# Kernel optimization log

Hardware: AMD Instinct MI355X
Metric: run time of the kernel (lower is better)

Reference implementation:

```python
import jax, jax.numpy as jnp
import numpy as np
import math

N = 20000          # nodes (residues)
E = 640000         # edges
CS = 384           # c_s
CZ = 128           # c_z
CH = 16            # c_hidden
H = 8              # no_heads
PQK = 8            # no_qk_points == no_v_points (forced equal, see notes)
FS = 128           # scalar channels in feat_irreps
PIN = 16           # vector channels in feat_irreps
HC = H * CH        # 128
HPQ = H * PQK * 3  # 192
CZ4 = CZ // 4      # 32
OUT_IN = HC + 3 * H + H + H * CZ4  # 416 actual concat width
INF = 100000.0
EPS = 1e-8


def setup_inputs() -> dict:
    key = jax.random.key(0)
    ks = jax.random.split(key, 16)
    w = lambda k, i, o: (jax.random.normal(k, (i, o), jnp.float32) / np.float32(np.sqrt(i)))
    frame_s = jax.random.normal(ks[0], (N, CS), jnp.float32)
    tfn_t = jax.random.normal(ks[1], (N, FS + 3 * PIN), jnp.float32)
    z = jax.random.normal(ks[2], (E, CZ), jnp.float32)
    edge_index = jax.random.randint(ks[3], (2, E), 0, N)
    mask = jnp.ones((N,), jnp.float32)
    # Rigid transforms: proper-ish rotations via QR, translations
    rot, _ = jnp.linalg.qr(jax.random.normal(ks[4], (N, 3, 3), jnp.float32))
    trans = jax.random.normal(ks[5], (N, 3), jnp.float32)
    return {
        "frame_s": frame_s, "tfn_t": tfn_t, "z": z,
        "edge_index": edge_index, "mask": mask,
        "rot": rot, "trans": trans,
        "Wq": w(ks[6], CS, HC), "bq": jnp.zeros((HC,), jnp.float32),
        "Wk_s": w(ks[7], FS, HC), "Wk_v": w(ks[8], PIN, PQK),
        "Wqp": w(ks[9], CS, HPQ), "bqp": jnp.zeros((HPQ,), jnp.float32),
        "Wb": w(ks[10], CZ, H), "bb": jnp.zeros((H,), jnp.float32),
        "Wdz": w(ks[11], CZ, CZ4), "bdz": jnp.zeros((CZ4,), jnp.float32),
        # ipa_point_weights_init_: softplus(hw) == 1  =>  hw = log(e - 1)
        "head_weights": jnp.full((H,), np.float32(np.log(np.e - 1.0))),
        "Wout": w(ks[12], OUT_IN, CS), "bout": jnp.zeros((CS,), jnp.float32),
    }


def _segment_softmax(a, seg, n):
    # pyg-style numerically stable segment softmax over edges grouped by seg
    m = jax.ops.segment_max(a, seg, num_segments=n)
    m = jnp.where(jnp.isfinite(m), m, 0.0)
    e = jnp.exp(a - m[seg])
    s = jax.ops.segment_sum(e, seg, num_segments=n)
    return e / (s[seg] + 1e-16)


def _forward(frame_s, tfn_t, z, mask, rot, trans,
             Wq, bq, Wk_s, Wk_v, Wqp, bqp, Wb, bb, Wdz, bdz,
             head_weights, Wout, bout, edge_index):
    n = frame_s.shape[0]
    src = edge_index[1]
    dst = edge_index[0]

    # scalar queries: [N,H,C]
    q = (frame_s @ Wq + bq).reshape(n, H, CH)

    # o3.Linear (feat_irreps -> k_irreps): scalars mix scalars, vectors mix vectors.
    # NOTE: original code uses linear_k for BOTH k and v (faithful bug), so v==k.
    scal = tfn_t[:, :FS]
    vecs = tfn_t[:, FS:].reshape(n, PIN, 3)
    k_scal = scal @ Wk_s                                   # [N, HC]
    k_vec = jnp.einsum('npx,pq->nqx', vecs, Wk_v)          # [N, PQK, 3]
    k = k_scal.reshape(n, H, CH)
    v = k
    k_tail = k_vec.reshape(n, PQK * 3)                     # [N, 24]
    # torch: split([3]*PQK) then stack(dim=-1) -> [N,3,PQK], then view [N,H,-1,3]
    k_pts = jnp.stack(jnp.split(k_tail, PQK, axis=-1), axis=-1)  # [N,3,PQK]
    k_pts = k_pts.reshape(n, H, -1, 3)                     # [N,H,1,3]
    v_pts = k_pts

    # query points, rigid-transformed: [N,H,PQK,3]
    q_pts = frame_s @ Wqp + bqp                            # [N, 3*H*PQK]
    q_pts = jnp.stack(jnp.split(q_pts, 3, axis=-1), axis=-1)  # [N, H*PQK, 3]
    q_pts = jnp.einsum('nij,npj->npi', rot, q_pts) + trans[:, None, :]
    q_pts = q_pts.reshape(n, H, PQK, 3)

    # scalar attention logits [E,H]
    a = jnp.einsum('ehc,ehc->eh', q[src], k[dst])
    a = a * np.float32(math.sqrt(1.0 / (3 * CH)))
    b = z @ Wb + bb                                        # [E,H]
    a = a + np.float32(math.sqrt(1.0 / 3)) * b

    # point attention: disp [E,H,PQK,3] (k_pts broadcasts over points)
    disp = q_pts[src] - k_pts[dst]
    pt_att = jnp.sum(disp * disp, axis=-1)                 # [E,H,PQK]
    hw = jax.nn.softplus(head_weights) * np.float32(math.sqrt(1.0 / (3 * (PQK * 9.0 / 2))))
    pt_att = -0.5 * jnp.sum(pt_att * hw[None, :, None], axis=-1)  # [E,H]

    edge_mask = INF * (mask[dst] * mask[src] - 1.0)        # [E]
    a = a + pt_att + edge_mask[:, None]

    a = _segment_softmax(a, src, n)                        # [E,H]

    # scalar output
    o = jax.ops.segment_sum(a[..., None] * v[dst], src, num_segments=n)  # [N,H,C]
    o = o.reshape(n, HC)

    # point output
    o_pt = jax.ops.segment_sum(a[:, :, None, None] * v_pts[dst], src, num_segments=n)  # [N,H,1,3]
    o_pt = jnp.einsum('nji,nhpj->nhpi', rot, o_pt - trans[:, None, None, :])  # invert_apply
    o_pt_norm = jnp.sqrt(jnp.sum(o_pt * o_pt, axis=-1) + EPS).reshape(n, H)
    o_pt = o_pt.reshape(n, -1, 3)                          # [N,H,3]

    # pair output
    pair_z = z @ Wdz + bdz                                 # [E,CZ4]
    o_pair = jax.ops.segment_sum(a[..., None] * pair_z[:, None, :], src, num_segments=n)  # [N,H,CZ4]
    o_pair = o_pair.reshape(n, H * CZ4)

    feats = jnp.concatenate(
        [o, o_pt[..., 0], o_pt[..., 1], o_pt[..., 2], o_pt_norm, o_pair], axis=-1)  # [N,416]
    return feats @ Wout + bout                             # [N, CS]


def reference(frame_s, tfn_t, z, edge_index, mask, rot, trans,
              Wq, bq, Wk_s, Wk_v, Wqp, bqp, Wb, bb, Wdz, bdz,
              head_weights, Wout, bout):
    return _forward(frame_s, tfn_t, z, mask, rot, trans,
                    Wq, bq, Wk_s, Wk_v, Wqp, bqp, Wb, bb, Wdz, bdz,
                    head_weights, Wout, bout, edge_index)
```

## Files before the change

### kernel.cpp

```cpp
#include <hip/hip_runtime.h>
#include <math.h>

typedef __attribute__((ext_vector_type(8))) short short8;
typedef __attribute__((ext_vector_type(4))) float f32x4;

static __device__ inline unsigned short f2bf(float f) {
    union { float f; unsigned u; } v; v.f = f;
    unsigned r = v.u + 0x7FFF + ((v.u >> 16) & 1);
    return (unsigned short)(r >> 16);
}

template<int WJ, bool GATHER>
__global__ __launch_bounds__(256) void gemm_mfma(
    const float* __restrict__ A, int lda,
    const int* __restrict__ gidx,
    const float* __restrict__ BT, int ldb,
    const float* __restrict__ bias,
    float* __restrict__ C, int ldc,
    int M, int N, int K)
{
    constexpr int GBN = WJ * 32;
    __shared__ unsigned short As[128 * 72];
    __shared__ unsigned short Bs[GBN * 72];

    const int t = threadIdx.x;
    const int wid = t >> 6, lane = t & 63;
    const int wm = (wid & 1) * 64;
    const int wn = (wid >> 1) * (WJ * 16);
    const int row16 = lane & 15, quad = lane >> 4;
    const int bm = blockIdx.x * 128;
    const int bn = blockIdx.y * GBN;

    f32x4 acc[4][WJ];
    #pragma unroll
    for (int i = 0; i < 4; ++i)
        #pragma unroll
        for (int j = 0; j < WJ; ++j)
            #pragma unroll
            for (int r = 0; r < 4; ++r) acc[i][j][r] = 0.f;

    const int ktiles = (K + 63) >> 6;
    for (int kt = 0; kt < ktiles; ++kt) {
        const int k0 = kt << 6;
        #pragma unroll
        for (int it = 0; it < 8; ++it) {
            int f = it * 256 + t;
            int row = f >> 4, kq = (f & 15) << 2;
            float4 av = make_float4(0.f, 0.f, 0.f, 0.f);
            if (bm + row < M && k0 + kq < K) {
                size_t ar;
                if constexpr (GATHER) ar = (size_t)gidx[bm + row];
                else                  ar = (size_t)(bm + row);
                av = *(const float4*)(A + ar * lda + k0 + kq);
            }
            ushort4 uv;
            uv.x = f2bf(av.x); uv.y = f2bf(av.y); uv.z = f2bf(av.z); uv.w = f2bf(av.w);
            *(ushort4*)(&As[row * 72 + kq]) = uv;
        }
        #pragma unroll
        for (int it = 0; it < WJ * 2; ++it) {
            int f = it * 256 + t;
            int row = f >> 4, kq = (f & 15) << 2;
            float4 bv = make_float4(0.f, 0.f, 0.f, 0.f);
            if (bn + row < N && k0 + kq < K)
                bv = *(const float4*)(BT + (size_t)(bn + row) * ldb + k0 + kq);
            ushort4 uv;
            uv.x = f2bf(bv.x); uv.y = f2bf(bv.y); uv.z = f2bf(bv.z); uv.w = f2bf(bv.w);
            *(ushort4*)(&Bs[row * 72 + kq]) = uv;
        }
        __syncthreads();

        #pragma unroll
        for (int ks = 0; ks < 64; ks += 32) {
            short8 af[4], bfv[WJ];
            #pragma unroll
            for (int i = 0; i < 4; ++i)
                af[i] = *(const short8*)(&As[(wm + i * 16 + row16) * 72 + ks + quad * 8]);
            #pragma unroll
            for (int j = 0; j < WJ; ++j)
                bfv[j] = *(const short8*)(&Bs[(wn + j * 16 + row16) * 72 + ks + quad * 8]);
            #pragma unroll
            for (int i = 0; i < 4; ++i)
                #pragma unroll
                for (int j = 0; j < WJ; ++j)
                    acc[i][j] = __builtin_amdgcn_mfma_f32_16x16x32_bf16(af[i], bfv[j], acc[i][j], 0, 0, 0);
        }
        __syncthreads();
    }

    #pragma unroll
    for (int i = 0; i < 4; ++i)
        #pragma unroll
        for (int j = 0; j < WJ; ++j) {
            int col = bn + wn + j * 16 + row16;
            if (col >= N) continue;
            float bv = bias ? bias[col] : 0.f;
            #pragma unroll
            for (int r = 0; r < 4; ++r) {
                int row = bm + wm + i * 16 + quad * 4 + r;
                if (row < M) C[(size_t)row * ldc + col] = acc[i][j][r] + bv;
            }
        }
}

__global__ void prep_kernel(const float* __restrict__ Wq, const float* __restrict__ bq,
                            const float* __restrict__ Wqp, const float* __restrict__ bqp,
                            const float* __restrict__ Wb, const float* __restrict__ bb,
                            const float* __restrict__ Wdz, const float* __restrict__ bdz,
                            const float* __restrict__ Wks, const float* __restrict__ Wout,
                            float* __restrict__ wqqpT, float* __restrict__ bqqp,
                            float* __restrict__ wcatT, float* __restrict__ bcat,
                            float* __restrict__ wksT, float* __restrict__ woutT,
                            int* __restrict__ cnt, int n)
{
    const float SC_QK = 0.14433756729740643f;
    const float SC_B  = 0.5773502691896258f;
    int gid = blockIdx.x * 256 + threadIdx.x;
    int stride = gridDim.x * 256;
    for (int i = gid; i < n; i += stride) cnt[i] = 0;
    for (int i = gid; i < 320 * 384; i += stride) {
        int o = i / 384, c = i % 384;
        wqqpT[i] = (o < 128) ? Wq[c * 128 + o] * SC_QK : Wqp[c * 192 + (o - 128)];
    }
    for (int i = gid; i < 320; i += stride) bqqp[i] = (i < 128) ? bq[i] * SC_QK : bqp[i - 128];
    for (int i = gid; i < 40 * 128; i += stride) {
        int o = i >> 7, c = i & 127;
        wcatT[i] = (o < 8) ? Wb[c * 8 + o] * SC_B : Wdz[c * 32 + (o - 8)];
    }
    for (int i = gid; i < 40; i += stride) bcat[i] = (i < 8) ? bb[i] * SC_B : bdz[i - 8];
    for (int i = gid; i < 128 * 128; i += stride) {
        int o = i >> 7, c = i & 127;
        wksT[i] = Wks[c * 128 + o];
    }
    for (int i = gid; i < 384 * 416; i += stride) {
        int o = i / 416, c = i % 416;
        woutT[i] = Wout[c * 384 + o];
    }
}

__global__ void kpts_kernel(const float* __restrict__ tfn, const float* __restrict__ Wkv,
                            float* __restrict__ kpts, int n)
{
    int t = blockIdx.x * 256 + threadIdx.x;
    if (t >= n * 24) return;
    int node = t / 24, f = t % 24;
    int a = f >> 3;
    int b = f & 7;
    const float* vr = tfn + (size_t)node * 176 + 128;
    float s = 0.f;
    #pragma unroll
    for (int p = 0; p < 16; ++p) s += vr[p * 3 + a] * Wkv[p * 8 + b];
    kpts[t] = s;
}

__global__ void qpts_kernel(const float* __restrict__ qpraw, const float* __restrict__ rot,
                            const float* __restrict__ trans, float* __restrict__ qpts, int n)
{
    int t = blockIdx.x * 256 + threadIdx.x;
    if (t >= n * 64) return;
    int node = t / 64, hk = t % 64;
    const float* qr = qpraw + (size_t)node * 320;
    float r0 = qr[hk], r1 = qr[64 + hk], r2 = qr[128 + hk];
    const float* R = rot + (size_t)node * 9;
    const float* T = trans + (size_t)node * 3;
    float* o = qpts + (size_t)node * 192 + hk * 3;
    #pragma unroll
    for (int i = 0; i < 3; ++i)
        o[i] = R[i * 3 + 0] * r0 + R[i * 3 + 1] * r1 + R[i * 3 + 2] * r2 + T[i];
}

__global__ void count_kernel(const int* __restrict__ srcA, int* __restrict__ cnt, int E)
{
    int e = blockIdx.x * 256 + threadIdx.x;
    if (e < E) atomicAdd(&cnt[srcA[e]], 1);
}

__global__ void scan_kernel(const int* __restrict__ cnt, int* __restrict__ off,
                            int* __restrict__ cur, int n)
{
    __shared__ int sums[1024];
    int t = threadIdx.x;
    int chunk = (n + 1023) >> 10;
    int begin = t * chunk;
    int local = 0;
    for (int j = 0; j < chunk; ++j) {
        int i = begin + j;
        if (i < n) local += cnt[i];
    }
    sums[t] = local;
    __syncthreads();
    for (int d = 1; d < 1024; d <<= 1) {
        int x = sums[t];
        int y = (t >= d) ? sums[t - d] : 0;
        __syncthreads();
        sums[t] = x + y;
        __syncthreads();
    }
    int run = sums[t] - local;
    for (int j = 0; j < chunk; ++j) {
        int i = begin + j;
        if (i < n) {
            off[i] = run;
            cur[i] = run;
            run += cnt[i];
        }
    }
}

__global__ void fill_kernel(const int* __restrict__ srcA, const int* __restrict__ dstA,
                            int* __restrict__ cur, int* __restrict__ elist,
                            int* __restrict__ dsts, int E)
{
    int e = blockIdx.x * 256 + threadIdx.x;
    if (e < E) {
        int s = srcA[e];
        int pos = atomicAdd(&cur[s], 1);
        elist[pos] = e;
        dsts[pos] = dstA[e];
    }
}

__global__ __launch_bounds__(256) void attn_kernel(
    const int* __restrict__ off, const int* __restrict__ cnt,
    const int* __restrict__ dsts,
    const float* __restrict__ qqp, const float* __restrict__ kbuf,
    const float* __restrict__ qpts, const float* __restrict__ kpts,
    const float* __restrict__ bpair, const float* __restrict__ mask,
    const float* __restrict__ hwin,
    const float* __restrict__ rot, const float* __restrict__ trans,
    float* __restrict__ feats, int n)
{
    int wave = threadIdx.x >> 6;
    int lane = threadIdx.x & 63;
    int s = blockIdx.x * 4 + wave;
    if (s >= n) return;
    int es = lane >> 3;
    int h  = lane & 7;

    float qh[16];
    {
        const float* qp = qqp + (size_t)s * 320 + h * 16;
        #pragma unroll
        for (int c = 0; c < 16; ++c) qh[c] = qp[c];
    }
    float qpt[24];
    {
        const float* pp = qpts + (size_t)s * 192 + h * 24;
        #pragma unroll
        for (int j = 0; j < 24; ++j) qpt[j] = pp[j];
    }
    float hwv = log1pf(__expf(hwin[h])) * 0.04811252243246882f;
    float mask_s = mask[s];
    int myoff = off[s], mycnt = cnt[s];

    float ssum = 0.f;
    float oacc[16];
    #pragma unroll
    for (int c = 0; c < 16; ++c) oacc[c] = 0.f;
    float optacc[3] = {0.f, 0.f, 0.f};
    float opacc[8][4];
    #pragma unroll
    for (int j = 0; j < 8; ++j)
        #pragma unroll
        for (int c = 0; c < 4; ++c) opacc[j][c] = 0.f;

    int nb = (mycnt + 7) >> 3;
    for (int b = 0; b < nb; ++b) {
        int idx = b * 8 + es;
        bool valid = idx < mycnt;
        int pos = myoff + (valid ? idx : 0);
        int d = dsts[pos];

        const float* bp = bpair + (size_t)pos * 40;
        float bh = bp[h];
        float4 pair4 = *(const float4*)(bp + 8 + h * 4);

        const float* kr = kbuf + (size_t)d * 128 + h * 16;
        float4 ka = *(const float4*)(kr + 0);
        float4 kb = *(const float4*)(kr + 4);
        float4 kc = *(const float4*)(kr + 8);
        float4 kd = *(const float4*)(kr + 12);

        const float* kp = kpts + (size_t)d * 24 + h * 3;
        float kp0 = kp[0], kp1 = kp[1], kp2 = kp[2];

        float qk = qh[0] * ka.x + qh[1] * ka.y + qh[2] * ka.z + qh[3] * ka.w
                 + qh[4] * kb.x + qh[5] * kb.y + qh[6] * kb.z + qh[7] * kb.w
                 + qh[8] * kc.x + qh[9] * kc.y + qh[10] * kc.z + qh[11] * kc.w
                 + qh[12] * kd.x + qh[13] * kd.y + qh[14] * kd.z + qh[15] * kd.w;

        float pt = 0.f;
        #pragma unroll
        for (int pp = 0; pp < 8; ++pp) {
            float d0 = qpt[pp * 3 + 0] - kp0;
            float d1 = qpt[pp * 3 + 1] - kp1;
            float d2 = qpt[pp * 3 + 2] - kp2;
            pt += d0 * d0 + d1 * d1 + d2 * d2;
        }

        float md = mask[d];
        float logit = qk + bh - hwv * pt + 100000.0f * (mask_s * md - 1.0f);
        float w = valid ? __expf(logit) : 0.f;

        ssum += w;
        oacc[0] += w * ka.x; oacc[1] += w * ka.y; oacc[2] += w * ka.z; oacc[3] += w * ka.w;
        oacc[4] += w * kb.x; oacc[5] += w * kb.y; oacc[6] += w * kb.z; oacc[7] += w * kb.w;
        oacc[8] += w * kc.x; oacc[9] += w * kc.y; oacc[10] += w * kc.z; oacc[11] += w * kc.w;
        oacc[12] += w * kd.x; oacc[13] += w * kd.y; oacc[14] += w * kd.z; oacc[15] += w * kd.w;
        optacc[0] += w * kp0;
        optacc[1] += w * kp1;
        optacc[2] += w * kp2;

        #pragma unroll
        for (int jh = 0; jh < 8; ++jh) {
            float wj = __shfl(w, (es << 3) + jh);
            opacc[jh][0] += wj * pair4.x;
            opacc[jh][1] += wj * pair4.y;
            opacc[jh][2] += wj * pair4.z;
            opacc[jh][3] += wj * pair4.w;
        }
    }

    #pragma unroll
    for (int delta = 8; delta <= 32; delta <<= 1) {
        ssum += __shfl_xor(ssum, delta);
        #pragma unroll
        for (int c = 0; c < 16; ++c) oacc[c] += __shfl_xor(oacc[c], delta);
        #pragma unroll
        for (int i = 0; i < 3; ++i) optacc[i] += __shfl_xor(optacc[i], delta);
        #pragma unroll
        for (int j = 0; j < 8; ++j)
            #pragma unroll
            for (int c = 0; c < 4; ++c) opacc[j][c] += __shfl_xor(opacc[j][c], delta);
    }

    float invj[8];
    #pragma unroll
    for (int jh = 0; jh < 8; ++jh)
        invj[jh] = 1.f / (__shfl(ssum, jh) + 1e-16f);

    if (es == 0) {
        float inv = 1.f / (ssum + 1e-16f);
        float* f = feats + (size_t)s * 416;
        #pragma unroll
        for (int c = 0; c < 16; c += 4) {
            float4 v = make_float4(oacc[c] * inv, oacc[c + 1] * inv, oacc[c + 2] * inv, oacc[c + 3] * inv);
            *(float4*)(&f[h * 16 + c]) = v;
        }
        const float* T = trans + (size_t)s * 3;
        const float* R = rot + (size_t)s * 9;
        float v0 = optacc[0] * inv - T[0];
        float v1 = optacc[1] * inv - T[1];
        float v2 = optacc[2] * inv - T[2];
        float r0 = R[0] * v0 + R[3] * v1 + R[6] * v2;
        float r1 = R[1] * v0 + R[4] * v1 + R[7] * v2;
        float r2 = R[2] * v0 + R[5] * v1 + R[8] * v2;
        f[128 + h] = r0;
        f[136 + h] = r1;
        f[144 + h] = r2;
        f[152 + h] = sqrtf(r0 * r0 + r1 * r1 + r2 * r2 + 1e-8f);
        #pragma unroll
        for (int jh = 0; jh < 8; ++jh) {
            float4 v = make_float4(opacc[jh][0] * invj[jh], opacc[jh][1] * invj[jh],
                                   opacc[jh][2] * invj[jh], opacc[jh][3] * invj[jh]);
            *(float4*)(&f[160 + jh * 32 + h * 4]) = v;
        }
    }
}

extern "C" void kernel_launch(void* const* d_in, const int* in_sizes, int n_in,
                              void* d_out, int out_size, void* d_ws, size_t ws_size,
                              hipStream_t stream)
{
    const float* frame_s = (const float*)d_in[0];
    const float* tfn     = (const float*)d_in[1];
    const float* z       = (const float*)d_in[2];
    const int*   ei      = (const int*)d_in[3];
    const float* mask    = (const float*)d_in[4];
    const float* rot     = (const float*)d_in[5];
    const float* trans   = (const float*)d_in[6];
    const float* Wq      = (const float*)d_in[7];
    const float* bq      = (const float*)d_in[8];
    const float* Wks     = (const float*)d_in[9];
    const float* Wkv     = (const float*)d_in[10];
    const float* Wqp     = (const float*)d_in[11];
    const float* bqp     = (const float*)d_in[12];
    const float* Wb      = (const float*)d_in[13];
    const float* bb      = (const float*)d_in[14];
    const float* Wdz     = (const float*)d_in[15];
    const float* bdz     = (const float*)d_in[16];
    const float* hw      = (const float*)d_in[17];
    const float* Wout    = (const float*)d_in[18];
    const float* bout    = (const float*)d_in[19];
    float* out = (float*)d_out;

    int n = in_sizes[0] / 384;
    int E = in_sizes[3] / 2;
    const int* dstA = ei;
    const int* srcA = ei + E;

    float* ws = (float*)d_ws;
    size_t p = 0;
    auto alloc = [&](size_t elems) -> float* {
        float* r = ws + p;
        p += (elems + 15) & ~((size_t)15);
        return r;
    };
    float* qqpbuf = alloc((size_t)n * 320);
    float* qpts   = alloc((size_t)n * 192);
    float* kbuf   = alloc((size_t)n * 128);
    float* kpts   = alloc((size_t)n * 24);
    float* feats  = alloc((size_t)n * 416);
    float* bpair  = alloc((size_t)E * 40);
    float* wqqpT  = alloc(320 * 384);
    float* bqqp   = alloc(320);
    float* wcatT  = alloc(40 * 128);
    float* bcat   = alloc(64);
    float* wksT   = alloc(128 * 128);
    float* woutT  = alloc(384 * 416);
    int* cnt   = (int*)alloc((size_t)n);
    int* off   = (int*)alloc((size_t)n);
    int* cur   = (int*)alloc((size_t)n);
    int* elist = (int*)alloc((size_t)E);
    int* dsts  = (int*)alloc((size_t)E);

    prep_kernel<<<512, 256, 0, stream>>>(Wq, bq, Wqp, bqp, Wb, bb, Wdz, bdz, Wks, Wout,
                                         wqqpT, bqqp, wcatT, bcat, wksT, woutT, cnt, n);

    count_kernel<<<(E + 255) / 256, 256, 0, stream>>>(srcA, cnt, E);
    scan_kernel<<<1, 1024, 0, stream>>>(cnt, off, cur, n);
    fill_kernel<<<(E + 255) / 256, 256, 0, stream>>>(srcA, dstA, cur, elist, dsts, E);

    {
        dim3 g((n + 127) / 128, 2);
        gemm_mfma<5, false><<<g, 256, 0, stream>>>(frame_s, 384, nullptr, wqqpT, 384, bqqp, qqpbuf, 320, n, 320, 384);
    }
    {
        dim3 g((n + 127) / 128, 1);
        gemm_mfma<4, false><<<g, 256, 0, stream>>>(tfn, 176, nullptr, wksT, 128, nullptr, kbuf, 128, n, 128, 128);
    }
    {
        dim3 g((E + 127) / 128, 1);
        gemm_mfma<2, true><<<g, 256, 0, stream>>>(z, 128, elist, wcatT, 128, bcat, bpair, 40, E, 40, 128);
    }
    kpts_kernel<<<(n * 24 + 255) / 256, 256, 0, stream>>>(tfn, Wkv, kpts, n);
    qpts_kernel<<<(n * 64 + 255) / 256, 256, 0, stream>>>(qqpbuf + 128, rot, trans, qpts, n);

    attn_kernel<<<(n + 3) / 4, 256, 0, stream>>>(off, cnt, dsts,
                                                 qqpbuf, kbuf, qpts, kpts, bpair, mask, hw,
                                                 rot, trans, feats, n);

    {
        dim3 g((n + 127) / 128, 2);
        gemm_mfma<6, false><<<g, 256, 0, stream>>>(feats, 416, nullptr, woutT, 416, bout, out, 384, n, 384, 416);
    }
    (void)n_in; (void)out_size; (void)ws_size;
}
```

Measured before the change: 966.7 us.

## Fuse independent projection GEMMs, kpts and CSR fill into one launch

Merges the edge-bias GEMM, q/qp GEMM, k GEMM, kpts and CSR fill kernels into a single block-partitioned launch so they run concurrently and the edge GEMM no longer waits on the fill. The edge GEMM now writes bpair in original edge order, and attention gathers it through elist instead of reading it contiguously. The qpts kernel and dsts buffer are removed: query points are rotated inline in attention, and destinations are read via dstA[e]. Tile widths also change (WJ=4 with more y-blocks). Attention gains an extra indirection and scattered bpair reads in exchange for fewer launches and less intermediate traffic.

```diff
diff --git a/kernel.cpp b/kernel.cpp
--- a/kernel.cpp
+++ b/kernel.cpp
@@ -10,26 +10,23 @@
     return (unsigned short)(r >> 16);
 }
 
-template<int WJ, bool GATHER>
-__global__ __launch_bounds__(256) void gemm_mfma(
+template<int WJ>
+__device__ __forceinline__ void gemm_body(
+    unsigned short* __restrict__ As, unsigned short* __restrict__ Bs,
     const float* __restrict__ A, int lda,
-    const int* __restrict__ gidx,
     const float* __restrict__ BT, int ldb,
     const float* __restrict__ bias,
     float* __restrict__ C, int ldc,
-    int M, int N, int K)
+    int M, int N, int K, int bx, int by)
 {
     constexpr int GBN = WJ * 32;
-    __shared__ unsigned short As[128 * 72];
-    __shared__ unsigned short Bs[GBN * 72];
-
     const int t = threadIdx.x;
     const int wid = t >> 6, lane = t & 63;
     const int wm = (wid & 1) * 64;
     const int wn = (wid >> 1) * (WJ * 16);
     const int row16 = lane & 15, quad = lane >> 4;
-    const int bm = blockIdx.x * 128;
-    const int bn = blockIdx.y * GBN;
+    const int bm = bx * 128;
+    const int bn = by * GBN;
 
     f32x4 acc[4][WJ];
     #pragma unroll
@@ -47,12 +44,8 @@
             int f = it * 256 + t;
             int row = f >> 4, kq = (f & 15) << 2;
             float4 av = make_float4(0.f, 0.f, 0.f, 0.f);
-            if (bm + row < M && k0 + kq < K) {
-                size_t ar;
-                if constexpr (GATHER) ar = (size_t)gidx[bm + row];
-                else                  ar = (size_t)(bm + row);
-                av = *(const float4*)(A + ar * lda + k0 + kq);
-            }
+            if (bm + row < M && k0 + kq < K)
+                av = *(const float4*)(A + (size_t)(bm + row) * lda + k0 + kq);
             ushort4 uv;
             uv.x = f2bf(av.x); uv.y = f2bf(av.y); uv.z = f2bf(av.z); uv.w = f2bf(av.w);
             *(ushort4*)(&As[row * 72 + kq]) = uv;
@@ -103,6 +96,74 @@
         }
 }
 
+template<int WJ>
+__global__ __launch_bounds__(256) void gemm_mfma(
+    const float* __restrict__ A, int lda,
+    const float* __restrict__ BT, int ldb,
+    const float* __restrict__ bias,
+    float* __restrict__ C, int ldc,
+    int M, int N, int K)
+{
+    __shared__ unsigned short As[128 * 72];
+    __shared__ unsigned short Bs[WJ * 32 * 72];
+    gemm_body<WJ>(As, Bs, A, lda, BT, ldb, bias, C, ldc, M, N, K, blockIdx.x, blockIdx.y);
+}
+
+__global__ __launch_bounds__(256) void mega_kernel(
+    const float* __restrict__ z, const float* __restrict__ wcatT,
+    const float* __restrict__ bcat, float* __restrict__ bpair, int E,
+    const float* __restrict__ frame_s, const float* __restrict__ wqqpT,
+    const float* __restrict__ bqqp, float* __restrict__ qqp, int n,
+    const float* __restrict__ tfn, const float* __restrict__ wksT,
+    float* __restrict__ kbuf,
+    const float* __restrict__ Wkv, float* __restrict__ kpts,
+    const int* __restrict__ srcA, int* __restrict__ cur, int* __restrict__ elist,
+    int nb_bp, int nb_qqp_x, int nb_qqp, int nb_k, int nb_kpts)
+{
+    __shared__ unsigned short As[128 * 72];
+    __shared__ unsigned short Bs[128 * 72];
+    int b = blockIdx.x;
+    if (b < nb_bp) {
+        gemm_body<2>(As, Bs, z, 128, wcatT, 128, bcat, bpair, 40, E, 40, 128, b, 0);
+        return;
+    }
+    b -= nb_bp;
+    if (b < nb_qqp) {
+        gemm_body<4>(As, Bs, frame_s, 384, wqqpT, 384, bqqp, qqp, 320, n, 320, 384,
+                     b % nb_qqp_x, b / nb_qqp_x);
+        return;
+    }
+    b -= nb_qqp;
+    if (b < nb_k) {
+        gemm_body<4>(As, Bs, tfn, 176, wksT, 128, nullptr, kbuf, 128, n, 128, 128, b, 0);
+        return;
+    }
+    b -= nb_k;
+    if (b < nb_kpts) {
+        int t = b * 256 + threadIdx.x;
+        if (t < n * 24) {
+            int node = t / 24, f = t % 24;
+            int a = f >> 3;
+            int bb2 = f & 7;
+            const float* vr = tfn + (size_t)node * 176 + 128;
+            float s = 0.f;
+            #pragma unroll
+            for (int p = 0; p < 16; ++p) s += vr[p * 3 + a] * Wkv[p * 8 + bb2];
+            kpts[t] = s;
+        }
+        return;
+    }
+    b -= nb_kpts;
+    {
+        int e = b * 256 + threadIdx.x;
+        if (e < E) {
+            int s = srcA[e];
+            int pos = atomicAdd(&cur[s], 1);
+            elist[pos] = e;
+        }
+    }
+}
+
 __global__ void prep_kernel(const float* __restrict__ Wq, const float* __restrict__ bq,
                             const float* __restrict__ Wqp, const float* __restrict__ bqp,
                             const float* __restrict__ Wb, const float* __restrict__ bb,
@@ -138,37 +199,6 @@
     }
 }
 
-__global__ void kpts_kernel(const float* __restrict__ tfn, const float* __restrict__ Wkv,
-                            float* __restrict__ kpts, int n)
-{
-    int t = blockIdx.x * 256 + threadIdx.x;
-    if (t >= n * 24) return;
-    int node = t / 24, f = t % 24;
-    int a = f >> 3;
-    int b = f & 7;
-    const float* vr = tfn + (size_t)node * 176 + 128;
-    float s = 0.f;
-    #pragma unroll
-    for (int p = 0; p < 16; ++p) s += vr[p * 3 + a] * Wkv[p * 8 + b];
-    kpts[t] = s;
-}
-
-__global__ void qpts_kernel(const float* __restrict__ qpraw, const float* __restrict__ rot,
-                            const float* __restrict__ trans, float* __restrict__ qpts, int n)
-{
-    int t = blockIdx.x * 256 + threadIdx.x;
-    if (t >= n * 64) return;
-    int node = t / 64, hk = t % 64;
-    const float* qr = qpraw + (size_t)node * 320;
-    float r0 = qr[hk], r1 = qr[64 + hk], r2 = qr[128 + hk];
-    const float* R = rot + (size_t)node * 9;
-    const float* T = trans + (size_t)node * 3;
-    float* o = qpts + (size_t)node * 192 + hk * 3;
-    #pragma unroll
-    for (int i = 0; i < 3; ++i)
-        o[i] = R[i * 3 + 0] * r0 + R[i * 3 + 1] * r1 + R[i * 3 + 2] * r2 + T[i];
-}
-
 __global__ void count_kernel(const int* __restrict__ srcA, int* __restrict__ cnt, int E)
 {
     int e = blockIdx.x * 256 + threadIdx.x;
@@ -207,24 +237,11 @@
     }
 }
 
-__global__ void fill_kernel(const int* __restrict__ srcA, const int* __restrict__ dstA,
-                            int* __restrict__ cur, int* __restrict__ elist,
-                            int* __restrict__ dsts, int E)
-{
-    int e = blockIdx.x * 256 + threadIdx.x;
-    if (e < E) {
-        int s = srcA[e];
-        int pos = atomicAdd(&cur[s], 1);
-        elist[pos] = e;
-        dsts[pos] = dstA[e];
-    }
-}
-
 __global__ __launch_bounds__(256) void attn_kernel(
     const int* __restrict__ off, const int* __restrict__ cnt,
-    const int* __restrict__ dsts,
+    const int* __restrict__ elist, const int* __restrict__ dstA,
     const float* __restrict__ qqp, const float* __restrict__ kbuf,
-    const float* __restrict__ qpts, const float* __restrict__ kpts,
+    const float* __restrict__ kpts,
     const float* __restrict__ bpair, const float* __restrict__ mask,
     const float* __restrict__ hwin,
     const float* __restrict__ rot, const float* __restrict__ trans,
@@ -243,11 +260,22 @@
         #pragma unroll
         for (int c = 0; c < 16; ++c) qh[c] = qp[c];
     }
+    const float* Rp = rot + (size_t)s * 9;
+    const float* Tp = trans + (size_t)s * 3;
+    float R0 = Rp[0], R1 = Rp[1], R2 = Rp[2];
+    float R3 = Rp[3], R4 = Rp[4], R5 = Rp[5];
+    float R6 = Rp[6], R7 = Rp[7], R8 = Rp[8];
+    float T0 = Tp[0], T1 = Tp[1], T2 = Tp[2];
     float qpt[24];
     {
-        const float* pp = qpts + (size_t)s * 192 + h * 24;
-        #pragma unroll
-        for (int j = 0; j < 24; ++j) qpt[j] = pp[j];
+        const float* qr = qqp + (size_t)s * 320 + 128 + h * 8;
+        #pragma unroll
+        for (int p2 = 0; p2 < 8; ++p2) {
+            float c0 = qr[p2], c1 = qr[64 + p2], c2 = qr[128 + p2];
+            qpt[p2 * 3 + 0] = R0 * c0 + R1 * c1 + R2 * c2 + T0;
+            qpt[p2 * 3 + 1] = R3 * c0 + R4 * c1 + R5 * c2 + T1;
+            qpt[p2 * 3 + 2] = R6 * c0 + R7 * c1 + R8 * c2 + T2;
+        }
     }
     float hwv = log1pf(__expf(hwin[h])) * 0.04811252243246882f;
     float mask_s = mask[s];
@@ -268,12 +296,8 @@
     for (int b = 0; b < nb; ++b) {
         int idx = b * 8 + es;
         bool valid = idx < mycnt;
-        int pos = myoff + (valid ? idx : 0);
-        int d = dsts[pos];
-
-        const float* bp = bpair + (size_t)pos * 40;
-        float bh = bp[h];
-        float4 pair4 = *(const float4*)(bp + 8 + h * 4);
+        int e = valid ? elist[myoff + idx] : 0;
+        int d = dstA[e];
 
         const float* kr = kbuf + (size_t)d * 128 + h * 16;
         float4 ka = *(const float4*)(kr + 0);
@@ -283,6 +307,10 @@
 
         const float* kp = kpts + (size_t)d * 24 + h * 3;
         float kp0 = kp[0], kp1 = kp[1], kp2 = kp[2];
+
+        const float* bp = bpair + (size_t)e * 40;
+        float bh = bp[h];
+        float4 pair4 = *(const float4*)(bp + 8 + h * 4);
 
         float qk = qh[0] * ka.x + qh[1] * ka.y + qh[2] * ka.z + qh[3] * ka.w
                  + qh[4] * kb.x + qh[5] * kb.y + qh[6] * kb.z + qh[7] * kb.w
@@ -347,14 +375,12 @@
             float4 v = make_float4(oacc[c] * inv, oacc[c + 1] * inv, oacc[c + 2] * inv, oacc[c + 3] * inv);
             *(float4*)(&f[h * 16 + c]) = v;
         }
-        const float* T = trans + (size_t)s * 3;
-        const float* R = rot + (size_t)s * 9;
-        float v0 = optacc[0] * inv - T[0];
-        float v1 = optacc[1] * inv - T[1];
-        float v2 = optacc[2] * inv - T[2];
-        float r0 = R[0] * v0 + R[3] * v1 + R[6] * v2;
-        float r1 = R[1] * v0 + R[4] * v1 + R[7] * v2;
-        float r2 = R[2] * v0 + R[5] * v1 + R[8] * v2;
+        float v0 = optacc[0] * inv - T0;
+        float v1 = optacc[1] * inv - T1;
+        float v2 = optacc[2] * inv - T2;
+        float r0 = R0 * v0 + R3 * v1 + R6 * v2;
+        float r1 = R1 * v0 + R4 * v1 + R7 * v2;
+        float r2 = R2 * v0 + R5 * v1 + R8 * v2;
         f[128 + h] = r0;
         f[136 + h] = r1;
         f[144 + h] = r2;
@@ -407,7 +433,6 @@
         return r;
     };
     float* qqpbuf = alloc((size_t)n * 320);
-    float* qpts   = alloc((size_t)n * 192);
     float* kbuf   = alloc((size_t)n * 128);
     float* kpts   = alloc((size_t)n * 24);
     float* feats  = alloc((size_t)n * 416);
@@ -422,37 +447,35 @@
     int* off   = (int*)alloc((size_t)n);
     int* cur   = (int*)alloc((size_t)n);
     int* elist = (int*)alloc((size_t)E);
-    int* dsts  = (int*)alloc((size_t)E);
 
     prep_kernel<<<512, 256, 0, stream>>>(Wq, bq, Wqp, bqp, Wb, bb, Wdz, bdz, Wks, Wout,
                                          wqqpT, bqqp, wcatT, bcat, wksT, woutT, cnt, n);
 
     count_kernel<<<(E + 255) / 256, 256, 0, stream>>>(srcA, cnt, E);
     scan_kernel<<<1, 1024, 0, stream>>>(cnt, off, cur, n);
-    fill_kernel<<<(E + 255) / 256, 256, 0, stream>>>(srcA, dstA, cur, elist, dsts, E);
+
+    int nb_bp    = (E + 127) / 128;
+    int nb_qqp_x = (n + 127) / 128;
+    int nb_qqp   = nb_qqp_x * 3;
+    int nb_k     = (n + 127) / 128;
+    int nb_kpts  = (n * 24 + 255) / 256;
+    int nb_fill  = (E + 255) / 256;
+    int nb_total = nb_bp + nb_qqp + nb_k + nb_kpts + nb_fill;
+    mega_kernel<<<nb_total, 256, 0, stream>>>(
+        z, wcatT, bcat, bpair, E,
+        frame_s, wqqpT, bqqp, qqpbuf, n,
+        tfn, wksT, kbuf,
+        Wkv, kpts,
+        srcA, cur, elist,
+        nb_bp, nb_qqp_x, nb_qqp, nb_k, nb_kpts);
+
+    attn_kernel<<<(n + 3) / 4, 256, 0, stream>>>(off, cnt, elist, dstA,
+                                                 qqpbuf, kbuf, kpts, bpair, mask, hw,
+                                                 rot, trans, feats, n);
 
     {
-        dim3 g((n + 127) / 128, 2);
-        gemm_mfma<5, false><<<g, 256, 0, stream>>>(frame_s, 384, nullptr, wqqpT, 384, bqqp, qqpbuf, 320, n, 320, 384);
-    }
-    {
-        dim3 g((n + 127) / 128, 1);
-        gemm_mfma<4, false><<<g, 256, 0, stream>>>(tfn, 176, nullptr, wksT, 128, nullptr, kbuf, 128, n, 128, 128);
-    }
-    {
-        dim3 g((E + 127) / 128, 1);
-        gemm_mfma<2, true><<<g, 256, 0, stream>>>(z, 128, elist, wcatT, 128, bcat, bpair, 40, E, 40, 128);
-    }
-    kpts_kernel<<<(n * 24 + 255) / 256, 256, 0, stream>>>(tfn, Wkv, kpts, n);
-    qpts_kernel<<<(n * 64 + 255) / 256, 256, 0, stream>>>(qqpbuf + 128, rot, trans, qpts, n);
-
-    attn_kernel<<<(n + 3) / 4, 256, 0, stream>>>(off, cnt, dsts,
-                                                 qqpbuf, kbuf, qpts, kpts, bpair, mask, hw,
-                                                 rot, trans, feats, n);
-
-    {
-        dim3 g((n + 127) / 128, 2);
-        gemm_mfma<6, false><<<g, 256, 0, stream>>>(feats, 416, nullptr, woutT, 416, bout, out, 384, n, 384, 416);
+        dim3 g((n + 127) / 128, 3);
+        gemm_mfma<4><<<g, 256, 0, stream>>>(feats, 416, woutT, 416, bout, out, 384, n, 384, 416);
     }
     (void)n_in; (void)out_size; (void)ws_size;
 }
```

Measured after the change: 914.2 us. -5.4%, faster.
